# Kernel optimization log

Measured on AMD Instinct MI355X. Metric: run time of the kernel, lower is better.

The kernel has to match this reference:

```python
import jax, jax.numpy as jnp
import numpy as np

INPUT_DIM = 784
HIDDEN = 4096
BATCH = 64
T = 30                      # time_steps
TAU = 100.0                 # tau_mem
DECAY = 1.0 - 1.0 / TAU     # LIF leak per step
THR = 0.5                   # spike threshold
SCALE = 16.0                # input_scale
K = int(HIDDEN * 0.08)      # k-WTA k = hidden_dim * sparsity = 327


def setup_inputs() -> dict:
    key = jax.random.key(0)
    k1, k2, k3 = jax.random.split(key, 3)
    x = jax.random.uniform(k1, (BATCH, INPUT_DIM), dtype=jnp.float32)
    W1 = jax.random.normal(k2, (INPUT_DIM, HIDDEN), dtype=jnp.float32) * 0.05
    W2 = jax.random.normal(k3, (HIDDEN, HIDDEN), dtype=jnp.float32) * 0.02
    return {"x": x, "W1": W1, "W2": W2}


def _kwta(s):
    # k-WTA: keep units >= k-th largest value per row (binary spikes -> this
    # matches torch.topk kth-value thresholding; if row sum==0 it's a no-op).
    vals = jax.lax.top_k(s, K)[0]           # [B, K]
    thresh = vals[:, -1:]                   # [B, 1]
    return s * (s >= thresh).astype(s.dtype)


def _lif(v, cur):
    # Leaky integrate-and-fire: decay, integrate, hard-threshold, reset-to-zero.
    v = v * DECAY + cur
    s = (v >= THR).astype(v.dtype)
    return v * (1.0 - s), s


def reference(x, W1, W2):
    # prepare_input: normalize by max and scale (x.max()>0 branch)
    x = x / jnp.maximum(jnp.max(x), jnp.float32(1e-12)) * SCALE
    B = x.shape[0]

    def step(carry, _):
        v0, v1, v2, sum0, sum1, sum2 = carry
        v0, s0 = _lif(v0, x)                # Retina: external current each step
        v1, s1 = _lif(v1, s0 @ W1)          # V1 feedforward
        v2, s2 = _lif(v2, s1 @ W2)          # V2 feedforward
        s1m = _kwta(s1)                     # k-WTA applied to returned spikes
        s2m = _kwta(s2)
        return (v0, v1, v2, sum0 + s0, sum1 + s1m, sum2 + s2m), None

    z0 = jnp.zeros((B, INPUT_DIM), jnp.float32)
    zh = jnp.zeros((B, HIDDEN), jnp.float32)
    carry = (z0, zh, zh, z0, zh, zh)
    (_, _, _, sum0, sum1, sum2), _ = jax.lax.scan(step, carry, None, length=T)
    # mean firing rates per group (spike_sums / time_steps)
    return (sum0 / T, sum1 / T, sum2 / T)
```

## Files before the change

kernel.cpp:

```cpp
#include <hip/hip_runtime.h>
#include <cstdint>
#include <cstddef>

#define INPUT_DIM 784
#define HIDDEN    4096
#define BATCH     64
#define T_STEPS   30
#define N0 (BATCH*INPUT_DIM)
#define N1 (BATCH*HIDDEN)
#define M_ROWS (T_STEPS*BATCH)
#define NDIG 4
#define MB_CNT (M_ROWS/32)
#define KC1 25
#define KC2 128

typedef int v4i  __attribute__((ext_vector_type(4)));
typedef int v16i __attribute__((ext_vector_type(16)));

__global__ __launch_bounds__(256) void max_kernel(const float* __restrict__ x,
                                                  unsigned* __restrict__ maxbits) {
    int i = blockIdx.x * 256 + threadIdx.x;
    float v = (i < N0) ? x[i] : 0.0f;
    #pragma unroll
    for (int off = 32; off > 0; off >>= 1)
        v = fmaxf(v, __shfl_down(v, off, 64));
    __shared__ float sm[4];
    int lane = threadIdx.x & 63;
    int wv   = threadIdx.x >> 6;
    if (lane == 0) sm[wv] = v;
    __syncthreads();
    if (threadIdx.x == 0) {
        float m = fmaxf(fmaxf(sm[0], sm[1]), fmaxf(sm[2], sm[3]));
        atomicMax(maxbits, __float_as_uint(m));
    }
}

__global__ __launch_bounds__(256) void lif0_kernel(const float* __restrict__ x,
                                                   const unsigned* __restrict__ maxbits,
                                                   uint8_t* __restrict__ AF1,
                                                   float* __restrict__ out0) {
    int j = blockIdx.x * 256 + threadIdx.x;
    int b = blockIdx.y;
    if (j >= INPUT_DIM) return;
    float mx = fmaxf(__uint_as_float(*maxbits), 1e-12f);
    float xs = __fmul_rn(__fdiv_rn(x[b * INPUT_DIM + j], mx), 16.0f);
    int kc = j >> 5;
    int lane = (b & 31) | (((j >> 4) & 1) << 5);
    size_t base = (((size_t)(kc * MB_CNT + (b >> 5)) * 64 + lane) << 4) + (j & 15);
    float v = 0.0f;
    int cnt = 0;
    #pragma unroll
    for (int t = 0; t < T_STEPS; ++t) {
        v = __fadd_rn(__fmul_rn(v, 0.99f), xs);
        int s = (v >= 0.5f) ? 1 : 0;
        cnt += s;
        v = s ? 0.0f : v;
        AF1[base + (size_t)t * 2048] = (uint8_t)s;
    }
    out0[b * INPUT_DIM + j] = (float)cnt / 30.0f;
}

__global__ __launch_bounds__(256) void digitize_kernel(const float* __restrict__ W,
                                                       int8_t* __restrict__ BF,
                                                       int Krows, int KC, double scale) {
    __shared__ float tile[32][33];
    const int nb = blockIdx.x, kc = blockIdx.y;
    const int tid = threadIdx.x;
    {
        int r  = tid >> 3;
        int c4 = (tid & 7) << 2;
        int k  = kc * 32 + r;
        float4 w4 = make_float4(0.f, 0.f, 0.f, 0.f);
        if (k < Krows)
            w4 = *(const float4*)&W[(size_t)k * HIDDEN + nb * 32 + c4];
        tile[r][c4]     = w4.x;
        tile[r][c4 + 1] = w4.y;
        tile[r][c4 + 2] = w4.z;
        tile[r][c4 + 3] = w4.w;
    }
    __syncthreads();
    const int d    = tid >> 6;
    const int lane = tid & 63;
    const int nl   = lane & 31;
    const int kh   = (lane >> 5) << 4;
    char dig[16];
    #pragma unroll
    for (int jj = 0; jj < 16; ++jj) {
        double w = (double)tile[kh + jj][nl];
        long long q = __double2ll_rn(w * scale);
        int dd = 0;
        #pragma unroll
        for (int dd_i = 0; dd_i <= 3; ++dd_i) {
            dd = (int)(((q + 128) & 255) - 128);
            q = (q - (long long)dd) >> 8;
            if (dd_i == d) break;
        }
        dig[jj] = (char)dd;
    }
    *(int4*)&BF[((((size_t)nb * KC + kc) * NDIG + d) << 10) + (lane << 4)] =
        *(int4*)&dig[0];
}

#define MFMA_GRP(A0, A1, B0, B1, B2, B3)                                        \
    acc[0][0] = __builtin_amdgcn_mfma_i32_32x32x32_i8(A0, B0, acc[0][0], 0, 0, 0); \
    acc[1][0] = __builtin_amdgcn_mfma_i32_32x32x32_i8(A1, B0, acc[1][0], 0, 0, 0); \
    acc[0][1] = __builtin_amdgcn_mfma_i32_32x32x32_i8(A0, B1, acc[0][1], 0, 0, 0); \
    acc[1][1] = __builtin_amdgcn_mfma_i32_32x32x32_i8(A1, B1, acc[1][1], 0, 0, 0); \
    acc[0][2] = __builtin_amdgcn_mfma_i32_32x32x32_i8(A0, B2, acc[0][2], 0, 0, 0); \
    acc[1][2] = __builtin_amdgcn_mfma_i32_32x32x32_i8(A1, B2, acc[1][2], 0, 0, 0); \
    acc[0][3] = __builtin_amdgcn_mfma_i32_32x32x32_i8(A0, B3, acc[0][3], 0, 0, 0); \
    acc[1][3] = __builtin_amdgcn_mfma_i32_32x32x32_i8(A1, B3, acc[1][3], 0, 0, 0)

template <int KC>
__global__ __launch_bounds__(256, 2) void gemm_i8_kernel(const int8_t* __restrict__ AF,
                                                         const int8_t* __restrict__ BF,
                                                         double* __restrict__ C,
                                                         double scale) {
    const int tid  = threadIdx.x;
    const int wave = tid >> 6, lane = tid & 63;
    const int i  = blockIdx.x;
    const int bx = i >> 6;
    const int by = ((i & 7) << 3) | ((i >> 3) & 7);
    const int nb  = by * 2 + (wave & 1);
    const int msb = (wave >> 1) * 2;
    const int mb0 = bx * 4 + msb;

    const int8_t* ap = AF + (((size_t)mb0 * 64 + lane) << 4);
    const int8_t* bp = BF + (((size_t)nb * KC * NDIG) << 10) + (lane << 4);
    const int astride = MB_CNT * 64 * 16;
    const int bstride = NDIG * 1024;

    v16i acc[2][4] = {};
    v4i As[2][2], Bs[2][4];

    As[0][0] = *(const v4i*)ap;          As[0][1] = *(const v4i*)(ap + 1024);
    Bs[0][0] = *(const v4i*)bp;          Bs[0][1] = *(const v4i*)(bp + 1024);
    Bs[0][2] = *(const v4i*)(bp + 2048); Bs[0][3] = *(const v4i*)(bp + 3072);
    ap += astride; bp += bstride;
    As[1][0] = *(const v4i*)ap;          As[1][1] = *(const v4i*)(ap + 1024);
    Bs[1][0] = *(const v4i*)bp;          Bs[1][1] = *(const v4i*)(bp + 1024);
    Bs[1][2] = *(const v4i*)(bp + 2048); Bs[1][3] = *(const v4i*)(bp + 3072);

    #pragma unroll 2
    for (int kc = 0; kc < KC - 2; ++kc) {
        const int s = kc & 1;
        ap += astride; bp += bstride;
        v4i na0 = *(const v4i*)ap;          v4i na1 = *(const v4i*)(ap + 1024);
        v4i nb0 = *(const v4i*)bp;          v4i nb1 = *(const v4i*)(bp + 1024);
        v4i nb2 = *(const v4i*)(bp + 2048); v4i nb3 = *(const v4i*)(bp + 3072);
        MFMA_GRP(As[s][0], As[s][1], Bs[s][0], Bs[s][1], Bs[s][2], Bs[s][3]);
        As[s][0] = na0; As[s][1] = na1;
        Bs[s][0] = nb0; Bs[s][1] = nb1; Bs[s][2] = nb2; Bs[s][3] = nb3;
    }
    {
        constexpr int s = (KC - 2) & 1;
        MFMA_GRP(As[s][0], As[s][1], Bs[s][0], Bs[s][1], Bs[s][2], Bs[s][3]);
        MFMA_GRP(As[s ^ 1][0], As[s ^ 1][1], Bs[s ^ 1][0], Bs[s ^ 1][1], Bs[s ^ 1][2], Bs[s ^ 1][3]);
    }

    const int col = lane & 31;
    const int rb  = (lane >> 5) << 2;
    const int n_g = by * 64 + (wave & 1) * 32 + col;
    #pragma unroll
    for (int s = 0; s < 2; ++s) {
        const int m_base = bx * 128 + (msb + s) * 32;
        #pragma unroll
        for (int r = 0; r < 16; ++r) {
            int row = (r & 3) + 8 * (r >> 2) + rb;
            long long v = 0;
            #pragma unroll
            for (int d = 3; d >= 0; --d) v = (v << 8) + (long long)acc[s][d][r];
            C[(size_t)(m_base + row) * HIDDEN + n_g] = (double)v * scale;
        }
    }
}

__global__ __launch_bounds__(256) void lif1_kernel(const double* __restrict__ CUR,
                                                   uint8_t* __restrict__ AF,
                                                   float* __restrict__ out1) {
    int e = blockIdx.x * 256 + threadIdx.x;
    int b = e >> 12;
    int j = e & 4095;
    int kc = j >> 5;
    int lane = (b & 31) | (((j >> 4) & 1) << 5);
    size_t base = (((size_t)(kc * MB_CNT + (b >> 5)) * 64 + lane) << 4) + (j & 15);
    double v = 0.0;
    int cnt = 0;
    #pragma unroll
    for (int t = 0; t < T_STEPS; ++t) {
        double cur = CUR[(size_t)t * N1 + e];
        v = __dadd_rn(__dmul_rn(v, 0.99), cur);
        int s = (v >= 0.5) ? 1 : 0;
        cnt += s;
        v = s ? 0.0 : v;
        AF[base + (size_t)t * 2048] = (uint8_t)s;
    }
    out1[e] = (float)cnt / 30.0f;
}

__global__ __launch_bounds__(256) void lif2_kernel(const double* __restrict__ CUR,
                                                   float* __restrict__ out2) {
    int e = blockIdx.x * 256 + threadIdx.x;
    double v = 0.0;
    int cnt = 0;
    #pragma unroll
    for (int t = 0; t < T_STEPS; ++t) {
        double cur = CUR[(size_t)t * N1 + e];
        v = __dadd_rn(__dmul_rn(v, 0.99), cur);
        int s = (v >= 0.5) ? 1 : 0;
        cnt += s;
        v = s ? 0.0 : v;
    }
    out2[e] = (float)cnt / 30.0f;
}

extern "C" void kernel_launch(void* const* d_in, const int* in_sizes, int n_in,
                              void* d_out, int out_size, void* d_ws, size_t ws_size,
                              hipStream_t stream) {
    const float* x  = (const float*)d_in[0];
    const float* W1 = (const float*)d_in[1];
    const float* W2 = (const float*)d_in[2];
    float* out = (float*)d_out;
    char*  ws  = (char*)d_ws;

    const size_t AF1_SZ = (size_t)KC1 * MB_CNT * 1024;
    const size_t BF1_SZ = (size_t)128 * KC1 * NDIG * 1024;
    const size_t AF2_SZ = (size_t)KC2 * MB_CNT * 1024;
    const size_t BF2_SZ = (size_t)128 * KC2 * NDIG * 1024;
    unsigned* maxbits = (unsigned*)ws;
    uint8_t*  AF1 = (uint8_t*)(ws + 256);
    int8_t*   BF1 = (int8_t*)(AF1 + AF1_SZ);
    uint8_t*  AF2 = (uint8_t*)(BF1 + BF1_SZ);
    int8_t*   BF2 = (int8_t*)(AF2 + AF2_SZ);
    double*   CURd = (double*)((char*)BF2 + BF2_SZ);

    float* out0 = out;
    float* out1 = out + N0;
    float* out2 = out + N0 + N1;

    hipMemsetAsync(maxbits, 0, 4, stream);
    hipMemsetAsync(AF1, 0, AF1_SZ, stream);
    max_kernel <<<(N0 + 255) / 256, 256, 0, stream>>>(x, maxbits);
    lif0_kernel<<<dim3(4, BATCH), 256, 0, stream>>>(x, maxbits, AF1, out0);
    digitize_kernel<<<dim3(128, KC1), 256, 0, stream>>>(W1, BF1, INPUT_DIM, KC1,
                                                        4294967296.0);
    digitize_kernel<<<dim3(128, KC2), 256, 0, stream>>>(W2, BF2, HIDDEN, KC2,
                                                        8589934592.0);
    gemm_i8_kernel<KC1><<<960, 256, 0, stream>>>((const int8_t*)AF1, BF1, CURd,
                                                 2.3283064365386963e-10);
    lif1_kernel<<<N1 / 256, 256, 0, stream>>>(CURd, AF2, out1);
    gemm_i8_kernel<KC2><<<960, 256, 0, stream>>>((const int8_t*)AF2, BF2, CURd,
                                                 1.1641532182693481e-10);
    lif2_kernel<<<N1 / 256, 256, 0, stream>>>(CURd, out2);
}
```

Before: 337.5 us.

## Triple-buffer int8 GEMM loads, remap blocks per XCD, batch digitize per block

The int8 MFMA GEMM moves from a double-buffered register prefetch to a three-stage one. K chunks are padded to a multiple of three, with zero padding added to the A buffers through an extra memset, so loads stay further ahead of the MFMAs. The block-to-tile mapping is rewritten so each XCD handles a contiguous group of N tiles in phases, which should improve L2 reuse of B. The weight digitize kernel now processes 128 rows per block and emits all four digits per element instead of recomputing the digit per wave. The cost is extra padded K work in both GEMMs and more registers held for the deeper buffering.

```diff
diff --git a/kernel.cpp b/kernel.cpp
--- a/kernel.cpp
+++ b/kernel.cpp
@@ -11,8 +11,11 @@
 #define M_ROWS (T_STEPS*BATCH)
 #define NDIG 4
 #define MB_CNT (M_ROWS/32)
-#define KC1 25
-#define KC2 128
+#define ACH 61440
+#define KCP1 27
+#define KCA1 28
+#define KCP2 129
+#define KCA2 132
 
 typedef int v4i  __attribute__((ext_vector_type(4)));
 typedef int v16i __attribute__((ext_vector_type(16)));
@@ -62,14 +65,15 @@
 
 __global__ __launch_bounds__(256) void digitize_kernel(const float* __restrict__ W,
                                                        int8_t* __restrict__ BF,
-                                                       int Krows, int KC, double scale) {
-    __shared__ float tile[32][33];
-    const int nb = blockIdx.x, kc = blockIdx.y;
+                                                       int Krows, int KCA, double scale) {
+    __shared__ float tile[128][33];
+    const int nb = blockIdx.x, kb = blockIdx.y;
     const int tid = threadIdx.x;
-    {
-        int r  = tid >> 3;
+    #pragma unroll
+    for (int p = 0; p < 4; ++p) {
+        int r  = p * 32 + (tid >> 3);
         int c4 = (tid & 7) << 2;
-        int k  = kc * 32 + r;
+        int k  = kb * 128 + r;
         float4 w4 = make_float4(0.f, 0.f, 0.f, 0.f);
         if (k < Krows)
             w4 = *(const float4*)&W[(size_t)k * HIDDEN + nb * 32 + c4];
@@ -79,84 +83,86 @@
         tile[r][c4 + 3] = w4.w;
     }
     __syncthreads();
-    const int d    = tid >> 6;
+    const int kcq  = tid >> 6;
     const int lane = tid & 63;
     const int nl   = lane & 31;
     const int kh   = (lane >> 5) << 4;
-    char dig[16];
+    char dig[4][16];
     #pragma unroll
     for (int jj = 0; jj < 16; ++jj) {
-        double w = (double)tile[kh + jj][nl];
-        long long q = __double2ll_rn(w * scale);
-        int dd = 0;
+        double wv = (double)tile[kcq * 32 + kh + jj][nl];
+        long long q = __double2ll_rn(wv * scale);
         #pragma unroll
-        for (int dd_i = 0; dd_i <= 3; ++dd_i) {
-            dd = (int)(((q + 128) & 255) - 128);
+        for (int d = 0; d < 4; ++d) {
+            int dd = (int)(((q + 128) & 255) - 128);
             q = (q - (long long)dd) >> 8;
-            if (dd_i == d) break;
+            dig[d][jj] = (char)dd;
         }
-        dig[jj] = (char)dd;
-    }
-    *(int4*)&BF[((((size_t)nb * KC + kc) * NDIG + d) << 10) + (lane << 4)] =
-        *(int4*)&dig[0];
-}
-
-#define MFMA_GRP(A0, A1, B0, B1, B2, B3)                                        \
-    acc[0][0] = __builtin_amdgcn_mfma_i32_32x32x32_i8(A0, B0, acc[0][0], 0, 0, 0); \
-    acc[1][0] = __builtin_amdgcn_mfma_i32_32x32x32_i8(A1, B0, acc[1][0], 0, 0, 0); \
-    acc[0][1] = __builtin_amdgcn_mfma_i32_32x32x32_i8(A0, B1, acc[0][1], 0, 0, 0); \
-    acc[1][1] = __builtin_amdgcn_mfma_i32_32x32x32_i8(A1, B1, acc[1][1], 0, 0, 0); \
-    acc[0][2] = __builtin_amdgcn_mfma_i32_32x32x32_i8(A0, B2, acc[0][2], 0, 0, 0); \
-    acc[1][2] = __builtin_amdgcn_mfma_i32_32x32x32_i8(A1, B2, acc[1][2], 0, 0, 0); \
-    acc[0][3] = __builtin_amdgcn_mfma_i32_32x32x32_i8(A0, B3, acc[0][3], 0, 0, 0); \
-    acc[1][3] = __builtin_amdgcn_mfma_i32_32x32x32_i8(A1, B3, acc[1][3], 0, 0, 0)
-
-template <int KC>
+    }
+    const int kc = kb * 4 + kcq;
+    #pragma unroll
+    for (int d = 0; d < 4; ++d)
+        *(int4*)&BF[((((size_t)nb * KCA + kc) * NDIG + d) << 10) + (lane << 4)] =
+            *(int4*)&dig[d][0];
+}
+
+#define MFMA_GRP(s)                                                                  \
+    acc[0][0] = __builtin_amdgcn_mfma_i32_32x32x32_i8(As[s][0], Bs[s][0], acc[0][0], 0, 0, 0); \
+    acc[1][0] = __builtin_amdgcn_mfma_i32_32x32x32_i8(As[s][1], Bs[s][0], acc[1][0], 0, 0, 0); \
+    acc[0][1] = __builtin_amdgcn_mfma_i32_32x32x32_i8(As[s][0], Bs[s][1], acc[0][1], 0, 0, 0); \
+    acc[1][1] = __builtin_amdgcn_mfma_i32_32x32x32_i8(As[s][1], Bs[s][1], acc[1][1], 0, 0, 0); \
+    acc[0][2] = __builtin_amdgcn_mfma_i32_32x32x32_i8(As[s][0], Bs[s][2], acc[0][2], 0, 0, 0); \
+    acc[1][2] = __builtin_amdgcn_mfma_i32_32x32x32_i8(As[s][1], Bs[s][2], acc[1][2], 0, 0, 0); \
+    acc[0][3] = __builtin_amdgcn_mfma_i32_32x32x32_i8(As[s][0], Bs[s][3], acc[0][3], 0, 0, 0); \
+    acc[1][3] = __builtin_amdgcn_mfma_i32_32x32x32_i8(As[s][1], Bs[s][3], acc[1][3], 0, 0, 0)
+
+#define LOADC(s)                                                        \
+    Bs[s][0] = *(const v4i*)bp;          Bs[s][1] = *(const v4i*)(bp + 1024); \
+    Bs[s][2] = *(const v4i*)(bp + 2048); Bs[s][3] = *(const v4i*)(bp + 3072); \
+    As[s][0] = *(const v4i*)ap;          As[s][1] = *(const v4i*)(ap + 1024); \
+    ap += ACH; bp += NDIG * 1024
+
+#define BODY(s)                                                         \
+    {                                                                   \
+        v4i t0 = *(const v4i*)bp;          v4i t1 = *(const v4i*)(bp + 1024); \
+        v4i t2 = *(const v4i*)(bp + 2048); v4i t3 = *(const v4i*)(bp + 3072); \
+        v4i t4 = *(const v4i*)ap;          v4i t5 = *(const v4i*)(ap + 1024); \
+        ap += ACH; bp += NDIG * 1024;                                   \
+        MFMA_GRP(s);                                                    \
+        Bs[s][0] = t0; Bs[s][1] = t1; Bs[s][2] = t2; Bs[s][3] = t3;     \
+        As[s][0] = t4; As[s][1] = t5;                                   \
+    }
+
+template <int KCA, int KCP>
 __global__ __launch_bounds__(256, 2) void gemm_i8_kernel(const int8_t* __restrict__ AF,
                                                          const int8_t* __restrict__ BF,
                                                          double* __restrict__ C,
                                                          double scale) {
     const int tid  = threadIdx.x;
     const int wave = tid >> 6, lane = tid & 63;
-    const int i  = blockIdx.x;
-    const int bx = i >> 6;
-    const int by = ((i & 7) << 3) | ((i >> 3) & 7);
+    const int i     = blockIdx.x;
+    const int xcd   = i & 7;
+    const int local = i >> 3;
+    const int phase = local / 60;
+    const int w     = local - phase * 60;
+    const int bx    = w >> 2;
+    const int by    = (xcd << 3) | (phase << 2) | (w & 3);
     const int nb  = by * 2 + (wave & 1);
     const int msb = (wave >> 1) * 2;
     const int mb0 = bx * 4 + msb;
 
     const int8_t* ap = AF + (((size_t)mb0 * 64 + lane) << 4);
-    const int8_t* bp = BF + (((size_t)nb * KC * NDIG) << 10) + (lane << 4);
-    const int astride = MB_CNT * 64 * 16;
-    const int bstride = NDIG * 1024;
+    const int8_t* bp = BF + (((size_t)nb * KCA * NDIG) << 10) + (lane << 4);
 
     v16i acc[2][4] = {};
-    v4i As[2][2], Bs[2][4];
-
-    As[0][0] = *(const v4i*)ap;          As[0][1] = *(const v4i*)(ap + 1024);
-    Bs[0][0] = *(const v4i*)bp;          Bs[0][1] = *(const v4i*)(bp + 1024);
-    Bs[0][2] = *(const v4i*)(bp + 2048); Bs[0][3] = *(const v4i*)(bp + 3072);
-    ap += astride; bp += bstride;
-    As[1][0] = *(const v4i*)ap;          As[1][1] = *(const v4i*)(ap + 1024);
-    Bs[1][0] = *(const v4i*)bp;          Bs[1][1] = *(const v4i*)(bp + 1024);
-    Bs[1][2] = *(const v4i*)(bp + 2048); Bs[1][3] = *(const v4i*)(bp + 3072);
-
-    #pragma unroll 2
-    for (int kc = 0; kc < KC - 2; ++kc) {
-        const int s = kc & 1;
-        ap += astride; bp += bstride;
-        v4i na0 = *(const v4i*)ap;          v4i na1 = *(const v4i*)(ap + 1024);
-        v4i nb0 = *(const v4i*)bp;          v4i nb1 = *(const v4i*)(bp + 1024);
-        v4i nb2 = *(const v4i*)(bp + 2048); v4i nb3 = *(const v4i*)(bp + 3072);
-        MFMA_GRP(As[s][0], As[s][1], Bs[s][0], Bs[s][1], Bs[s][2], Bs[s][3]);
-        As[s][0] = na0; As[s][1] = na1;
-        Bs[s][0] = nb0; Bs[s][1] = nb1; Bs[s][2] = nb2; Bs[s][3] = nb3;
-    }
-    {
-        constexpr int s = (KC - 2) & 1;
-        MFMA_GRP(As[s][0], As[s][1], Bs[s][0], Bs[s][1], Bs[s][2], Bs[s][3]);
-        MFMA_GRP(As[s ^ 1][0], As[s ^ 1][1], Bs[s ^ 1][0], Bs[s ^ 1][1], Bs[s ^ 1][2], Bs[s ^ 1][3]);
-    }
+    v4i As[3][2], Bs[3][4];
+
+    LOADC(0); LOADC(1); LOADC(2);
+
+    for (int kc = 0; kc < KCP - 3; kc += 3) {
+        BODY(0); BODY(1); BODY(2);
+    }
+    MFMA_GRP(0); MFMA_GRP(1); MFMA_GRP(2);
 
     const int col = lane & 31;
     const int rb  = (lane >> 5) << 2;
@@ -223,10 +229,10 @@
     float* out = (float*)d_out;
     char*  ws  = (char*)d_ws;
 
-    const size_t AF1_SZ = (size_t)KC1 * MB_CNT * 1024;
-    const size_t BF1_SZ = (size_t)128 * KC1 * NDIG * 1024;
-    const size_t AF2_SZ = (size_t)KC2 * MB_CNT * 1024;
-    const size_t BF2_SZ = (size_t)128 * KC2 * NDIG * 1024;
+    const size_t AF1_SZ = (size_t)KCP1 * ACH;
+    const size_t BF1_SZ = (size_t)128 * KCA1 * NDIG * 1024;
+    const size_t AF2_SZ = (size_t)KCP2 * ACH;
+    const size_t BF2_SZ = (size_t)128 * KCA2 * NDIG * 1024;
     unsigned* maxbits = (unsigned*)ws;
     uint8_t*  AF1 = (uint8_t*)(ws + 256);
     int8_t*   BF1 = (int8_t*)(AF1 + AF1_SZ);
@@ -240,16 +246,17 @@
 
     hipMemsetAsync(maxbits, 0, 4, stream);
     hipMemsetAsync(AF1, 0, AF1_SZ, stream);
+    hipMemsetAsync(AF2 + (size_t)128 * ACH, 0, ACH, stream);
     max_kernel <<<(N0 + 255) / 256, 256, 0, stream>>>(x, maxbits);
     lif0_kernel<<<dim3(4, BATCH), 256, 0, stream>>>(x, maxbits, AF1, out0);
-    digitize_kernel<<<dim3(128, KC1), 256, 0, stream>>>(W1, BF1, INPUT_DIM, KC1,
-                                                        4294967296.0);
-    digitize_kernel<<<dim3(128, KC2), 256, 0, stream>>>(W2, BF2, HIDDEN, KC2,
-                                                        8589934592.0);
-    gemm_i8_kernel<KC1><<<960, 256, 0, stream>>>((const int8_t*)AF1, BF1, CURd,
-                                                 2.3283064365386963e-10);
+    digitize_kernel<<<dim3(128, KCA1 / 4), 256, 0, stream>>>(W1, BF1, INPUT_DIM, KCA1,
+                                                             4294967296.0);
+    digitize_kernel<<<dim3(128, KCA2 / 4), 256, 0, stream>>>(W2, BF2, HIDDEN, KCA2,
+                                                             8589934592.0);
+    gemm_i8_kernel<KCA1, KCP1><<<960, 256, 0, stream>>>((const int8_t*)AF1, BF1, CURd,
+                                                        2.3283064365386963e-10);
     lif1_kernel<<<N1 / 256, 256, 0, stream>>>(CURd, AF2, out1);
-    gemm_i8_kernel<KC2><<<960, 256, 0, stream>>>((const int8_t*)AF2, BF2, CURd,
-                                                 1.1641532182693481e-10);
+    gemm_i8_kernel<KCA2, KCP2><<<960, 256, 0, stream>>>((const int8_t*)AF2, BF2, CURd,
+                                                        1.1641532182693481e-10);
     lif2_kernel<<<N1 / 256, 256, 0, stream>>>(CURd, out2);
 }
```

Result: slower. 345.4 us (+2.3%).
